# Performance work log

Hardware: AMD Instinct MI355X
Metric: run time of the kernel (lower is better)

## Reference

```python
import jax, jax.numpy as jnp
import numpy as np

B, L, D_MODEL = 2, 4096, 1024
D_INNER = 2048  # expand * d_model
D_CONV = 4


def setup_inputs() -> dict:
    key = jax.random.key(0)
    ks = jax.random.split(key, 7)
    return {
        "hidden_states": jax.random.normal(ks[0], (B, L, D_MODEL), jnp.float32),
        "W_in": jax.random.normal(ks[1], (2 * D_INNER, D_MODEL), jnp.float32) * 0.02,
        "conv_w": jax.random.normal(ks[2], (D_INNER, D_CONV), jnp.float32) * 0.1,
        "conv_b": jax.random.normal(ks[3], (D_INNER,), jnp.float32) * 0.1,
        "k_ssm": jax.random.normal(ks[4], (D_INNER, L), jnp.float32) * 0.02,  # materialized SSM kernel (channels=1)
        "D_skip": jax.random.normal(ks[5], (D_INNER,), jnp.float32),
        "W_out": jax.random.normal(ks[6], (D_MODEL, D_INNER), jnp.float32) * 0.02,
    }


def _silu(x):
    return x * jax.nn.sigmoid(x)


def reference(hidden_states, W_in, conv_w, conv_b, k_ssm, D_skip, W_out):
    Bq, Lq, _ = hidden_states.shape
    # in_proj (no bias): (B, L, d_model) -> (B, 2*d_inner, L)
    xz = jnp.einsum('bld,ed->bel', hidden_states, W_in)
    x, z = jnp.split(xz, 2, axis=1)  # each (B, d_inner, L)

    # causal depthwise conv1d (pad left d_conv-1) + SiLU (causal_conv1d_fn)
    xp = jnp.pad(x, ((0, 0), (0, 0), (D_CONV - 1, 0)))
    xc = conv_b[None, :, None]
    for j in range(D_CONV):
        xc = xc + conv_w[None, :, j, None] * xp[:, :, j:j + Lq]
    x = _silu(xc)

    # FFT long convolution (l_kernel = L, n = 2L), channels = 1
    n = 2 * Lq
    x_f = jnp.fft.rfft(x, n=n)            # (B, H, n//2+1) complex
    k_f = jnp.fft.rfft(k_ssm, n=n)        # (H, n//2+1)
    y = jnp.fft.irfft(x_f * k_f[None], n=n)[..., :Lq]  # (B, H, L)

    # D skip connection
    y = y + x * D_skip[None, :, None]

    # gating with SiLU(z)
    y = y * _silu(z)

    # out_proj (no bias): (B, H, L) -> (B, L, d_model)
    return jnp.einsum('bhl,dh->bld', y, W_out)
```

## Files before the change

### kernel.cpp

```cpp
#include <hip/hip_runtime.h>
#include <hip/hip_bf16.h>
#include <math.h>

#define B_SZ 2
#define L_SZ 4096
#define DM   1024
#define DI   2048
#define E_SZ 4096
#define DC   4

typedef unsigned short u16;
typedef __attribute__((ext_vector_type(8))) short short8;
typedef __attribute__((ext_vector_type(4))) float f32x4;

__device__ __forceinline__ float silu_f(float v) {
    return v / (1.0f + __expf(-v));
}

__device__ __forceinline__ void split_bf16(float x, u16& h, u16& l) {
    unsigned u  = __float_as_uint(x);
    unsigned hb = u & 0xFFFF0000u;
    h = (u16)(hb >> 16);
    float lf = x - __uint_as_float(hb);
    l = (u16)(__float_as_uint(lf) >> 16);
}
__device__ __forceinline__ float bf2f(u16 h) {
    return __uint_as_float(((unsigned)h) << 16);
}

__device__ __forceinline__ void gld_lds16(const u16* g, u16* l) {
    __builtin_amdgcn_global_load_lds(
        (const __attribute__((address_space(1))) unsigned int*)g,
        (__attribute__((address_space(3))) unsigned int*)l, 16, 0, 0);
}

__global__ __launch_bounds__(256) void pack_rm(
    const float* __restrict__ X, u16* __restrict__ H, u16* __restrict__ Lo,
    int ldx, int r16n, long sX, long sOut)
{
    const long cid = (long)blockIdx.x * 256 + threadIdx.x;
    const int  qc  = (int)(cid & 63);
    const long blk = cid >> 6;
    const int  r16 = (int)(blk % r16n);
    const int  k32 = (int)(blk / r16n);
    const int  q = qc >> 4, m = qc & 15;

    const float* src = X + blockIdx.y * sX + (long)(r16 * 16 + m) * ldx + k32 * 32 + q * 8;
    float4 v0 = *(const float4*)src;
    float4 v1 = *(const float4*)(src + 4);
    float v[8] = {v0.x,v0.y,v0.z,v0.w,v1.x,v1.y,v1.z,v1.w};

    u16 hs[8], ls[8];
    #pragma unroll
    for (int j = 0; j < 8; ++j) split_bf16(v[j], hs[j], ls[j]);

    const long o = blockIdx.y * sOut + cid * 8;
    *(uint4*)&H[o]  = *(const uint4*)hs;
    *(uint4*)&Lo[o] = *(const uint4*)ls;
}

__global__ __launch_bounds__(256) void gemm_mfma(
    const u16* __restrict__ Ah, const u16* __restrict__ Al,
    const u16* __restrict__ Bh, const u16* __restrict__ Bl,
    float* __restrict__ C,
    int r16A, int r16B, long sA, long sB, long sC,
    int ldc, int nk32)
{
    __shared__ alignas(16) u16 sm[4][4096];

    const int tid  = threadIdx.x;
    const int wv   = tid >> 6, lane = tid & 63;
    const long zb  = blockIdx.z;

    const u16* srcs0 = Ah + zb * sA;
    const u16* srcs1 = Al + zb * sA;
    const u16* srcs2 = Bh + zb * sB;
    const u16* srcs3 = Bl + zb * sB;
    const u16* mysrc = (wv == 0) ? srcs0 : (wv == 1) ? srcs1 : (wv == 2) ? srcs2 : srcs3;
    const int  rblk  = (wv < 2) ? blockIdx.x * 8 : blockIdx.y * 8;
    const int  r16c  = (wv < 2) ? r16A : r16B;
    u16* myl = sm[wv];

    const int wr = wv >> 1, wc = wv & 1;

    f32x4 acc[4][4];
    #pragma unroll
    for (int i = 0; i < 4; ++i)
        #pragma unroll
        for (int j = 0; j < 4; ++j)
            #pragma unroll
            for (int r = 0; r < 4; ++r) acc[i][j][r] = 0.f;

    for (int s = 0; s < nk32; ++s) {
        if (s) __syncthreads();
        {
            const u16* g = mysrc + (((long)s * r16c + rblk) << 9) + lane * 8;
            #pragma unroll
            for (int i = 0; i < 8; ++i)
                gld_lds16(g + (i << 9), myl + (i << 9));
        }
        __syncthreads();

        short8 afh[4], afl[4], bfh[4], bfl[4];
        const int aoff = (wr * 4) * 512 + lane * 8;
        const int boff = (wc * 4) * 512 + lane * 8;
        #pragma unroll
        for (int t = 0; t < 4; ++t) {
            afh[t] = *(const short8*)&sm[0][aoff + t * 512];
            afl[t] = *(const short8*)&sm[1][aoff + t * 512];
            bfh[t] = *(const short8*)&sm[2][boff + t * 512];
            bfl[t] = *(const short8*)&sm[3][boff + t * 512];
        }
        #pragma unroll
        for (int i = 0; i < 4; ++i)
            #pragma unroll
            for (int j = 0; j < 4; ++j) {
                acc[i][j] = __builtin_amdgcn_mfma_f32_16x16x32_bf16(afh[i], bfh[j], acc[i][j], 0, 0, 0);
                acc[i][j] = __builtin_amdgcn_mfma_f32_16x16x32_bf16(afh[i], bfl[j], acc[i][j], 0, 0, 0);
                acc[i][j] = __builtin_amdgcn_mfma_f32_16x16x32_bf16(afl[i], bfh[j], acc[i][j], 0, 0, 0);
            }
    }

    const int m_ = lane & 15, q_ = lane >> 4;
    float* Cb = C + zb * sC;
    const int row00 = blockIdx.x * 128 + wr * 64 + q_ * 4;
    const int col0  = blockIdx.y * 128 + wc * 64 + m_;
    #pragma unroll
    for (int i = 0; i < 4; ++i)
        #pragma unroll
        for (int j = 0; j < 4; ++j) {
            const long base = (long)(row00 + i * 16) * ldc + col0 + j * 16;
            #pragma unroll
            for (int r = 0; r < 4; ++r)
                Cb[base + (long)r * ldc] = acc[i][j][r];
        }
}

__global__ __launch_bounds__(256) void conv_silu_split(
    const float* __restrict__ xz, const float* __restrict__ conv_w,
    const float* __restrict__ conv_b,
    u16* __restrict__ xh_gl, u16* __restrict__ xl_gl)
{
    const long gid = (long)blockIdx.x * 256 + threadIdx.x;
    const int  q   = (int)(gid % (L_SZ / 4));
    const long bc  = gid / (L_SZ / 4);
    const int  ch  = (int)(bc % DI);
    const int  b   = (int)(bc / DI);

    const float* row = xz + ((long)b * E_SZ + ch) * L_SZ;
    const int l0 = q * 4;

    float4 cur  = *(const float4*)&row[l0];
    float4 prev = q ? *(const float4*)&row[l0 - 4] : make_float4(0.f, 0.f, 0.f, 0.f);

    const float w0 = conv_w[ch*DC+0], w1 = conv_w[ch*DC+1];
    const float w2 = conv_w[ch*DC+2], w3 = conv_w[ch*DC+3];
    const float bias = conv_b[ch];

    float o[4];
    o[0] = silu_f(bias + w0*prev.y + w1*prev.z + w2*prev.w + w3*cur.x);
    o[1] = silu_f(bias + w0*prev.z + w1*prev.w + w2*cur.x  + w3*cur.y);
    o[2] = silu_f(bias + w0*prev.w + w1*cur.x  + w2*cur.y  + w3*cur.z);
    o[3] = silu_f(bias + w0*cur.x  + w1*cur.y  + w2*cur.z  + w3*cur.w);

    unsigned long long hp = 0ull, lp = 0ull;
    #pragma unroll
    for (int r = 0; r < 4; ++r) {
        u16 h, l; split_bf16(o[r], h, l);
        hp |= ((unsigned long long)h) << (16*r);
        lp |= ((unsigned long long)l) << (16*r);
    }
    const long base = ((long)b * DI + ch) * L_SZ + l0;
    *(unsigned long long*)&xh_gl[base] = hp;
    *(unsigned long long*)&xl_gl[base] = lp;
}

__global__ __launch_bounds__(256) void pack_k(
    const float* __restrict__ k_ssm, unsigned* __restrict__ kv)
{
    const long gid = (long)blockIdx.x * 256 + threadIdx.x;
    const int  qq  = (int)(gid & (L_SZ / 4 - 1));
    const int  ch  = (int)(gid >> 10);

    const long off = ((long)ch << 12) + qq * 4;
    float4 v = *(const float4*)&k_ssm[off];
    float f[4] = { v.x, v.y, v.z, v.w };
    unsigned o[4];
    #pragma unroll
    for (int r = 0; r < 4; ++r) {
        u16 h, l; split_bf16(f[r], h, l);
        o[r] = (unsigned)h | ((unsigned)l << 16);
    }
    *(uint4*)&kv[off] = *(const uint4*)o;
}

__global__ __launch_bounds__(256, 6) void longconv_mfma(
    u16* __restrict__ xh_gl, u16* __restrict__ xl_gl,
    const float* __restrict__ xz,  const unsigned* __restrict__ kv,
    const float* __restrict__ D_skip)
{
    __shared__ alignas(16) u16 XH[4352];
    __shared__ alignas(16) u16 XL[4352];

    const int tid  = threadIdx.x;
    const int lane = tid & 63;
    const int wv   = tid >> 6;
    const int wc   = blockIdx.x;
    const int ch   = wc & (DI - 1);
    const int b    = wc >> 11;

    u16*            xhr = xh_gl + ((long)b * DI + ch) * L_SZ;
    u16*            xlr = xl_gl + ((long)b * DI + ch) * L_SZ;
    const unsigned* kvr = kv + ((long)ch << 12);

    if (tid < 64) {
        uint4 z = make_uint4(0u, 0u, 0u, 0u);
        ((uint4*)((tid < 32) ? XH : XL))[tid & 31] = z;
    }
    {
        const int ck = wv * 2;
        gld_lds16(xhr + (ck    ) * 512 + lane * 8, XH + 256 + (ck    ) * 512);
        gld_lds16(xhr + (ck + 1) * 512 + lane * 8, XH + 256 + (ck + 1) * 512);
        gld_lds16(xlr + (ck    ) * 512 + lane * 8, XL + 256 + (ck    ) * 512);
        gld_lds16(xlr + (ck + 1) * 512 + lane * 8, XL + 256 + (ck + 1) * 512);
    }
    __syncthreads();

    const int m_ = lane & 15;
    const int q_ = lane >> 4;
    const int dq = m_ - 8 * q_ + ((q_ >= 2) ? 32 : 0);
    const int xoff_lane = 256 + 16 * m_ + 8 * q_ - ((q_ >= 2) ? 32 : 0);

    const int tset[4] = { wv, 7 - wv, 8 + wv, 15 - wv };
    const int tmax = 15 - wv;
    const int cmax = 8 * tmax + 7;

    f32x4 acc[4];
    #pragma unroll
    for (int u = 0; u < 4; ++u)
        #pragma unroll
        for (int r = 0; r < 4; ++r) acc[u][r] = 0.f;

    const unsigned* kp = kvr + dq;

    unsigned lcur[8];
    #pragma unroll
    for (int e = 0; e < 8; ++e) {
        const int ki = dq - e;
        lcur[e] = (ki >= 0) ? kvr[ki] : 0u;
    }

    for (int c = 0; c <= cmax; ++c) {
        union { unsigned u[4]; short8 s; } Ah_, Al_;
        #pragma unroll
        for (int i = 0; i < 4; ++i) {
            Ah_.u[i] = __builtin_amdgcn_perm(lcur[2*i+1], lcur[2*i], 0x05040100u);
            Al_.u[i] = __builtin_amdgcn_perm(lcur[2*i+1], lcur[2*i], 0x07060302u);
        }
        const short8 ah = Ah_.s, al = Al_.s;

        unsigned lnext[8];
        if (c < cmax) {
            const int kb = 32 * (c + 1);
            #pragma unroll
            for (int e = 0; e < 8; ++e) lnext[e] = kp[kb - e];
        }

        const int xbase = xoff_lane - 32 * c;
        #pragma unroll
        for (int u = 0; u < 4; ++u) {
            const int t = tset[u];
            if (8 * t >= c - 7) {
                short8 bh = *(const short8*)&XH[xbase + 256 * t];
                short8 bl = *(const short8*)&XL[xbase + 256 * t];
                acc[u] = __builtin_amdgcn_mfma_f32_16x16x32_bf16(ah, bh, acc[u], 0, 0, 0);
                acc[u] = __builtin_amdgcn_mfma_f32_16x16x32_bf16(ah, bl, acc[u], 0, 0, 0);
                acc[u] = __builtin_amdgcn_mfma_f32_16x16x32_bf16(al, bh, acc[u], 0, 0, 0);
            }
        }

        if (c < cmax) {
            #pragma unroll
            for (int e = 0; e < 8; ++e) lcur[e] = lnext[e];
        }
    }

    const float  Ds   = D_skip[ch];
    const float* zrow = xz + ((long)b * E_SZ + DI + ch) * L_SZ;

    #pragma unroll
    for (int u = 0; u < 4; ++u) {
        const int t  = tset[u];
        const int l0 = 256 * t + 16 * m_ + 4 * q_;
        float4 zv = *(const float4*)&zrow[l0];
        float zt[4] = { zv.x, zv.y, zv.z, zv.w };
        unsigned long long hp = 0ull, lp = 0ull;
        #pragma unroll
        for (int r = 0; r < 4; ++r) {
            const float xf = bf2f(XH[256 + l0 + r]) + bf2f(XL[256 + l0 + r]);
            const float o  = (acc[u][r] + Ds * xf) * silu_f(zt[r]);
            u16 h, l; split_bf16(o, h, l);
            hp |= ((unsigned long long)h) << (16*r);
            lp |= ((unsigned long long)l) << (16*r);
        }
        *(unsigned long long*)&xhr[l0] = hp;
        *(unsigned long long*)&xlr[l0] = lp;
    }
}

__global__ __launch_bounds__(256) void pack_y(
    const u16* __restrict__ Yh, const u16* __restrict__ Yl,
    u16* __restrict__ OH, u16* __restrict__ OL, long sOut)
{
    __shared__ u16 T[2][32][136];
    const int t  = threadIdx.x;
    const int l0 = blockIdx.x * 128;
    const int h0 = blockIdx.y * 32;
    const int b  = blockIdx.z;

    const u16* yb_h = Yh + ((long)b * DI + h0) * L_SZ + l0;
    const u16* yb_l = Yl + ((long)b * DI + h0) * L_SZ + l0;

    #pragma unroll
    for (int i = 0; i < 2; ++i) {
        const int c = t + 256 * i;
        const int row = c >> 4, col = (c & 15) * 8;
        *(uint4*)&T[0][row][col] = *(const uint4*)&yb_h[(long)row * L_SZ + col];
        *(uint4*)&T[1][row][col] = *(const uint4*)&yb_l[(long)row * L_SZ + col];
    }
    __syncthreads();

    u16* outs[2] = { OH + b * sOut, OL + b * sOut };
    #pragma unroll
    for (int p = 0; p < 2; ++p) {
        #pragma unroll
        for (int i = 0; i < 2; ++i) {
            const int c = t + 256 * i;
            const int r16b = c >> 6, qc = c & 63;
            const int q = qc >> 4, m = qc & 15;
            const int l = r16b * 16 + m;
            u16 vals[8];
            #pragma unroll
            for (int j = 0; j < 8; ++j) vals[j] = T[p][q * 8 + j][l];
            const long o = ((long)(blockIdx.y * 256 + blockIdx.x * 8 + r16b) << 9) + qc * 8;
            *(uint4*)&outs[p][o] = *(const uint4*)vals;
        }
    }
}

extern "C" void kernel_launch(void* const* d_in, const int* in_sizes, int n_in,
                              void* d_out, int out_size, void* d_ws, size_t ws_size,
                              hipStream_t stream)
{
    const float* hidden = (const float*)d_in[0];
    const float* W_in   = (const float*)d_in[1];
    const float* conv_w = (const float*)d_in[2];
    const float* conv_b = (const float*)d_in[3];
    const float* k_ssm  = (const float*)d_in[4];
    const float* D_skip = (const float*)d_in[5];
    const float* W_out  = (const float*)d_in[6];
    float* out = (float*)d_out;

    char* ws = (char*)d_ws;
    float* xz  = (float*)ws;
    u16*   xh  = (u16*)(ws + 134217728);
    u16*   xl  = (u16*)(ws + 167772160);
    u16*   WinH  = (u16*)(ws + 201326592);
    u16*   WinL  = WinH + 4194304;
    u16*   WoutH = (u16*)(ws + 201326592);
    u16*   WoutL = WoutH + 2097152;
    u16*   hidH  = (u16*)(ws + 218103808);
    u16*   hidL  = hidH + 8388608;
    unsigned* klv = (unsigned*)ws;
    u16*   yAh   = (u16*)ws;
    u16*   yAl   = yAh + 8388608;

    pack_rm<<<dim3(2048, 1), 256, 0, stream>>>(W_in, WinH, WinL, DM, 256, 0L, 0L);
    pack_rm<<<dim3(2048, B_SZ), 256, 0, stream>>>(hidden, hidH, hidL, DM, 256,
        (long)L_SZ * DM, 4194304L);

    gemm_mfma<<<dim3(32, 32, B_SZ), 256, 0, stream>>>(
        WinH, WinL, hidH, hidL, xz,
        256, 256, 0L, 4194304L, (long)E_SZ * L_SZ, L_SZ, 32);

    conv_silu_split<<<dim3((unsigned)((long)B_SZ*DI*(L_SZ/4)/256)), 256, 0, stream>>>(
        xz, conv_w, conv_b, xh, xl);

    pack_k<<<dim3((unsigned)((long)DI * (L_SZ/4) / 256)), 256, 0, stream>>>(k_ssm, klv);

    longconv_mfma<<<dim3(B_SZ * DI), 256, 0, stream>>>(
        xh, xl, xz, klv, D_skip);

    pack_rm<<<dim3(1024, 1), 256, 0, stream>>>(W_out, WoutH, WoutL, DI, 64, 0L, 0L);

    pack_y<<<dim3(32, 64, B_SZ), 256, 0, stream>>>(
        xh, xl, yAh, yAl, 33554432L);

    gemm_mfma<<<dim3(32, 8, B_SZ), 256, 0, stream>>>(
        yAh, yAl, WoutH, WoutL, out,
        256, 64, 33554432L, 0L, (long)L_SZ * DM, DM, 64);
}
```

Baseline: 622.6 us.

## Pair adjacent output tiles per wave to reuse LDS x fragments in longconv

Restructures the MFMA Toeplitz long-convolution loop. Each wave now processes pairs of adjacent 256-wide output tiles (ta, ta+1) in two sweeps instead of four interleaved tiles. The x fragments loaded for tile ta at one chunk are kept in registers and reused for tile ta+1 eight chunks later, which roughly halves LDS reads. The k-fragment prefetch is unrolled with double buffering. Launch bounds drop from 6 to 4 waves per SIMD to allow for the extra registers, which may reduce occupancy.

```diff
diff --git a/kernel.cpp b/kernel.cpp
--- a/kernel.cpp
+++ b/kernel.cpp
@@ -32,6 +32,28 @@
     __builtin_amdgcn_global_load_lds(
         (const __attribute__((address_space(1))) unsigned int*)g,
         (__attribute__((address_space(3))) unsigned int*)l, 16, 0, 0);
+}
+
+__device__ __forceinline__ void mfma_triple(
+    f32x4& acc, short8 ah, short8 al, short8 bh, short8 bl)
+{
+    acc = __builtin_amdgcn_mfma_f32_16x16x32_bf16(ah, bh, acc, 0, 0, 0);
+    acc = __builtin_amdgcn_mfma_f32_16x16x32_bf16(ah, bl, acc, 0, 0, 0);
+    acc = __builtin_amdgcn_mfma_f32_16x16x32_bf16(al, bh, acc, 0, 0, 0);
+}
+
+__device__ __forceinline__ void kperm(const unsigned* cur, short8& ah, short8& al) {
+    union { unsigned u[4]; short8 s; } A_, B_;
+    #pragma unroll
+    for (int i = 0; i < 4; ++i) {
+        A_.u[i] = __builtin_amdgcn_perm(cur[2*i+1], cur[2*i], 0x05040100u);
+        B_.u[i] = __builtin_amdgcn_perm(cur[2*i+1], cur[2*i], 0x07060302u);
+    }
+    ah = A_.s; al = B_.s;
+}
+__device__ __forceinline__ void kpref(const unsigned* kp, int c1, unsigned* nxt) {
+    #pragma unroll
+    for (int e = 0; e < 8; ++e) nxt[e] = kp[32*c1 - e];
 }
 
 __global__ __launch_bounds__(256) void pack_rm(
@@ -194,7 +216,7 @@
     *(uint4*)&kv[off] = *(const uint4*)o;
 }
 
-__global__ __launch_bounds__(256, 6) void longconv_mfma(
+__global__ __launch_bounds__(256, 4) void longconv_mfma(
     u16* __restrict__ xh_gl, u16* __restrict__ xl_gl,
     const float* __restrict__ xz,  const unsigned* __restrict__ kv,
     const float* __restrict__ D_skip)
@@ -231,80 +253,88 @@
     const int dq = m_ - 8 * q_ + ((q_ >= 2) ? 32 : 0);
     const int xoff_lane = 256 + 16 * m_ + 8 * q_ - ((q_ >= 2) ? 32 : 0);
 
-    const int tset[4] = { wv, 7 - wv, 8 + wv, 15 - wv };
-    const int tmax = 15 - wv;
-    const int cmax = 8 * tmax + 7;
-
-    f32x4 acc[4];
-    #pragma unroll
-    for (int u = 0; u < 4; ++u)
-        #pragma unroll
-        for (int r = 0; r < 4; ++r) acc[u][r] = 0.f;
-
-    const unsigned* kp = kvr + dq;
-
-    unsigned lcur[8];
-    #pragma unroll
-    for (int e = 0; e < 8; ++e) {
-        const int ki = dq - e;
-        lcur[e] = (ki >= 0) ? kvr[ki] : 0u;
-    }
-
-    for (int c = 0; c <= cmax; ++c) {
-        union { unsigned u[4]; short8 s; } Ah_, Al_;
-        #pragma unroll
-        for (int i = 0; i < 4; ++i) {
-            Ah_.u[i] = __builtin_amdgcn_perm(lcur[2*i+1], lcur[2*i], 0x05040100u);
-            Al_.u[i] = __builtin_amdgcn_perm(lcur[2*i+1], lcur[2*i], 0x07060302u);
-        }
-        const short8 ah = Ah_.s, al = Al_.s;
-
-        unsigned lnext[8];
-        if (c < cmax) {
-            const int kb = 32 * (c + 1);
-            #pragma unroll
-            for (int e = 0; e < 8; ++e) lnext[e] = kp[kb - e];
-        }
-
-        const int xbase = xoff_lane - 32 * c;
-        #pragma unroll
-        for (int u = 0; u < 4; ++u) {
-            const int t = tset[u];
-            if (8 * t >= c - 7) {
-                short8 bh = *(const short8*)&XH[xbase + 256 * t];
-                short8 bl = *(const short8*)&XL[xbase + 256 * t];
-                acc[u] = __builtin_amdgcn_mfma_f32_16x16x32_bf16(ah, bh, acc[u], 0, 0, 0);
-                acc[u] = __builtin_amdgcn_mfma_f32_16x16x32_bf16(ah, bl, acc[u], 0, 0, 0);
-                acc[u] = __builtin_amdgcn_mfma_f32_16x16x32_bf16(al, bh, acc[u], 0, 0, 0);
+    const float     Ds   = D_skip[ch];
+    const float*    zrow = xz + ((long)b * E_SZ + DI + ch) * L_SZ;
+    const unsigned* kp   = kvr + dq;
+
+    for (int sw = 0; sw < 2; ++sw) {
+        const int ta    = sw ? (14 - 2 * wv) : (2 * wv);
+        const int tb    = ta + 1;
+        const int baseA = xoff_lane + 256 * ta;
+
+        f32x4 accA, accB;
+        #pragma unroll
+        for (int r = 0; r < 4; ++r) { accA[r] = 0.f; accB[r] = 0.f; }
+
+        unsigned kc[8], kn[8];
+        #pragma unroll
+        for (int e = 0; e < 8; ++e) {
+            const int ki = dq - e;
+            kc[e] = (ki >= 0) ? kvr[ki] : 0u;
+        }
+
+        short8 rh[8], rl[8];
+
+        #pragma unroll
+        for (int u = 0; u < 8; ++u) {
+            short8 ah, al;
+            if ((u & 1) == 0) { kperm(kc, ah, al); kpref(kp, u + 1, kn); }
+            else              { kperm(kn, ah, al); kpref(kp, u + 1, kc); }
+            const int xb = baseA - 32 * u;
+            rh[u] = *(const short8*)&XH[xb];
+            rl[u] = *(const short8*)&XL[xb];
+            short8 sbh = *(const short8*)&XH[xb + 256];
+            short8 sbl = *(const short8*)&XL[xb + 256];
+            mfma_triple(accA, ah, al, rh[u], rl[u]);
+            mfma_triple(accB, ah, al, sbh, sbl);
+        }
+
+        for (int c8 = 1; c8 <= ta; ++c8) {
+            #pragma unroll
+            for (int u = 0; u < 8; ++u) {
+                const int c = 8 * c8 + u;
+                short8 ah, al;
+                if ((u & 1) == 0) { kperm(kc, ah, al); kpref(kp, c + 1, kn); }
+                else              { kperm(kn, ah, al); kpref(kp, c + 1, kc); }
+                mfma_triple(accB, ah, al, rh[u], rl[u]);
+                const int xb = baseA - 32 * c;
+                rh[u] = *(const short8*)&XH[xb];
+                rl[u] = *(const short8*)&XL[xb];
+                mfma_triple(accA, ah, al, rh[u], rl[u]);
             }
         }
 
-        if (c < cmax) {
-            #pragma unroll
-            for (int e = 0; e < 8; ++e) lcur[e] = lnext[e];
-        }
-    }
-
-    const float  Ds   = D_skip[ch];
-    const float* zrow = xz + ((long)b * E_SZ + DI + ch) * L_SZ;
-
-    #pragma unroll
-    for (int u = 0; u < 4; ++u) {
-        const int t  = tset[u];
-        const int l0 = 256 * t + 16 * m_ + 4 * q_;
-        float4 zv = *(const float4*)&zrow[l0];
-        float zt[4] = { zv.x, zv.y, zv.z, zv.w };
-        unsigned long long hp = 0ull, lp = 0ull;
-        #pragma unroll
-        for (int r = 0; r < 4; ++r) {
-            const float xf = bf2f(XH[256 + l0 + r]) + bf2f(XL[256 + l0 + r]);
-            const float o  = (acc[u][r] + Ds * xf) * silu_f(zt[r]);
-            u16 h, l; split_bf16(o, h, l);
-            hp |= ((unsigned long long)h) << (16*r);
-            lp |= ((unsigned long long)l) << (16*r);
-        }
-        *(unsigned long long*)&xhr[l0] = hp;
-        *(unsigned long long*)&xlr[l0] = lp;
+        {
+            const int c0 = 8 * (ta + 1);
+            #pragma unroll
+            for (int u = 0; u < 8; ++u) {
+                const int c = c0 + u;
+                short8 ah, al;
+                if ((u & 1) == 0) { kperm(kc, ah, al); kpref(kp, c + 1, kn); }
+                else              { kperm(kn, ah, al); kpref(kp, c + 1, kc); }
+                mfma_triple(accB, ah, al, rh[u], rl[u]);
+            }
+        }
+
+        #pragma unroll
+        for (int u2 = 0; u2 < 2; ++u2) {
+            const int  t  = u2 ? tb : ta;
+            const f32x4 A = u2 ? accB : accA;
+            const int  l0 = 256 * t + 16 * m_ + 4 * q_;
+            float4 zv = *(const float4*)&zrow[l0];
+            float zt[4] = { zv.x, zv.y, zv.z, zv.w };
+            unsigned long long hp = 0ull, lp = 0ull;
+            #pragma unroll
+            for (int r = 0; r < 4; ++r) {
+                const float xf = bf2f(XH[256 + l0 + r]) + bf2f(XL[256 + l0 + r]);
+                const float o  = (A[r] + Ds * xf) * silu_f(zt[r]);
+                u16 h, l; split_bf16(o, h, l);
+                hp |= ((unsigned long long)h) << (16*r);
+                lp |= ((unsigned long long)l) << (16*r);
+            }
+            *(unsigned long long*)&xhr[l0] = hp;
+            *(unsigned long long*)&xlr[l0] = lp;
+        }
     }
 }
 
```

After: 768.2 us. 23.4% more time.
